# Kernel tuning notes

Measured on AMD Instinct MI355X. Metric: run time of the kernel, lower is better.

The kernel has to match this reference:

```python
import jax, jax.numpy as jnp
import numpy as np

B = 16384
DIM = 1024
HEADS = 16
LN_EPS = 1e-5


def setup_inputs() -> dict:
    key = jax.random.key(0)
    ks = jax.random.split(key, 8)
    d = DIM
    s = 0.02
    return {
        "x_u": jax.random.normal(ks[0], (B, d), dtype=jnp.float32),
        "x_m": jax.random.normal(ks[1], (B, d), dtype=jnp.float32),
        # MHA m2u (path 1): packed in_proj [3d, d] like torch, out_proj [d, d]
        "w_qkv1": (jax.random.normal(ks[2], (3 * d, d), dtype=jnp.float32) * s),
        "b_qkv1": jnp.zeros((3 * d,), dtype=jnp.float32),
        "w_o1": (jax.random.normal(ks[3], (d, d), dtype=jnp.float32) * s),
        "b_o1": jnp.zeros((d,), dtype=jnp.float32),
        # MHA u2m (path 2)
        "w_qkv2": (jax.random.normal(ks[4], (3 * d, d), dtype=jnp.float32) * s),
        "b_qkv2": jnp.zeros((3 * d,), dtype=jnp.float32),
        "w_o2": (jax.random.normal(ks[5], (d, d), dtype=jnp.float32) * s),
        "b_o2": jnp.zeros((d,), dtype=jnp.float32),
        # proj head: LayerNorm(2d) + Linear(2d -> d) + GELU (dropout = eval identity)
        "ln_g": jnp.ones((2 * d,), dtype=jnp.float32),
        "ln_b": jnp.zeros((2 * d,), dtype=jnp.float32),
        "w_proj": (jax.random.normal(ks[6], (d, 2 * d), dtype=jnp.float32) * s),
        "b_proj": jnp.zeros((d,), dtype=jnp.float32),
        "heads": HEADS,
    }


def _mha_single_token(xq, xkv, w_qkv, b_qkv, w_o, b_o, heads):
    # seq_len = 1 cross-attention: softmax over a single key is exactly 1.
    d = xq.shape[-1]
    dh = d // heads
    wq, wk, wv = jnp.split(w_qkv, 3, axis=0)
    bq, bk, bv = jnp.split(b_qkv, 3)
    q = (xq @ wq.T + bq).reshape(-1, heads, dh)   # [B, H, dh]
    k = (xkv @ wk.T + bk).reshape(-1, heads, dh)
    v = (xkv @ wv.T + bv).reshape(-1, heads, dh)
    scores = jnp.sum(q * k, axis=-1) / jnp.sqrt(jnp.asarray(dh, q.dtype))  # [B, H]
    attn = jax.nn.softmax(scores[..., None], axis=-1)  # singleton key axis -> ones
    out = (attn * v).reshape(-1, d)                    # [B, d]
    return out @ w_o.T + b_o


def reference(x_u, x_m, w_qkv1, b_qkv1, w_o1, b_o1,
              w_qkv2, b_qkv2, w_o2, b_o2,
              ln_g, ln_b, w_proj, b_proj, heads):
    # Path 1: Q = x_m, K/V = x_u ; Path 2: Q = x_u, K/V = x_m
    z1 = _mha_single_token(x_m, x_u, w_qkv1, b_qkv1, w_o1, b_o1, heads)
    z2 = _mha_single_token(x_u, x_m, w_qkv2, b_qkv2, w_o2, b_o2, heads)
    z = jnp.concatenate([z1, z2], axis=-1)  # [B, 2d]
    mu = jnp.mean(z, axis=-1, keepdims=True)
    var = jnp.mean(jnp.square(z - mu), axis=-1, keepdims=True)
    zn = (z - mu) * jax.lax.rsqrt(var + LN_EPS) * ln_g + ln_b
    h = zn @ w_proj.T + b_proj               # [B, d]
    return jax.nn.gelu(h, approximate=False)  # torch nn.GELU default = exact erf
```

## Files before the change

kernel.cpp:

```cpp
#include <hip/hip_runtime.h>
#include <cstdint>


#define DIM 1024
#define BROWS 16384

typedef __bf16 bf16x8 __attribute__((ext_vector_type(8)));
typedef float f32x4 __attribute__((ext_vector_type(4)));

__device__ __forceinline__ ushort f2bf(float f) {
    uint32_t u = __builtin_bit_cast(uint32_t, f);
    u = (u + 0x7fffu + ((u >> 16) & 1u)) >> 16;
    return (ushort)u;
}

__device__ __forceinline__ void async_copy16(const void* gsrc, void* ldst) {
    __builtin_amdgcn_global_load_lds(
        (__attribute__((address_space(1))) void*)((uintptr_t)gsrc),
        (__attribute__((address_space(3))) void*)((uint32_t)(uintptr_t)ldst),
        16, 0, 0);
}


__global__ __launch_bounds__(256) void prep_kernel(
        const float* __restrict__ x_u, const float* __restrict__ x_m,
        const float* __restrict__ wqkv1, const float* __restrict__ bqkv1,
        const float* __restrict__ wo1, const float* __restrict__ bo1,
        const float* __restrict__ wqkv2, const float* __restrict__ bqkv2,
        const float* __restrict__ wo2, const float* __restrict__ bo2,
        const float* __restrict__ lng, const float* __restrict__ lnb,
        const float* __restrict__ wproj, const float* __restrict__ bproj,
        ushort* __restrict__ x_bf, ushort* __restrict__ wo12,
        ushort* __restrict__ wvT12, ushort* __restrict__ Wp,
        float* __restrict__ b12, float* __restrict__ Svec, float* __restrict__ Cvec,
        float* __restrict__ sums ) {
    const int b = blockIdx.x, t = threadIdx.x;
    __shared__ float red[4][4];
    __shared__ float tls[32][33];

    if (b < 8192) {
        const int n4 = (BROWS * DIM) / 4;
        int i = b * 256 + t;
        const int stride = 8192 * 256;
        const float4* xu4 = (const float4*)x_u;
        const float4* xm4 = (const float4*)x_m;
        ushort4* o4 = (ushort4*)x_bf;
#pragma unroll
        for (int it = 0; it < 4; it++, i += stride) {
            float4 v = (i < n4) ? xu4[i] : xm4[i - n4];
            ushort4 o;
            o.x = f2bf(v.x); o.y = f2bf(v.y); o.z = f2bf(v.z); o.w = f2bf(v.w);
            o4[i] = o;
        }
    } else if (b < 9216) {
        int j = b - 8192;
        float s1 = 0.f, s2 = 0.f, sS = 0.f, sC = 0.f;
        for (int c = t; c < DIM; c += 256) {
            s1 += wo1[j * DIM + c] * bqkv1[2 * DIM + c];
            s2 += wo2[j * DIM + c] * bqkv2[2 * DIM + c];
        }
        for (int c = t; c < 2 * DIM; c += 256) {
            float w = wproj[j * 2 * DIM + c];
            sS += w * lng[c];
            sC += w * lnb[c];
        }
        for (int o = 32; o; o >>= 1) {
            s1 += __shfl_down(s1, o, 64);
            s2 += __shfl_down(s2, o, 64);
            sS += __shfl_down(sS, o, 64);
            sC += __shfl_down(sC, o, 64);
        }
        int wid = t >> 6;
        if ((t & 63) == 0) { red[wid][0] = s1; red[wid][1] = s2; red[wid][2] = sS; red[wid][3] = sC; }
        __syncthreads();
        if (t == 0) {
            s1 = red[0][0] + red[1][0] + red[2][0] + red[3][0];
            s2 = red[0][1] + red[1][1] + red[2][1] + red[3][1];
            sS = red[0][2] + red[1][2] + red[2][2] + red[3][2];
            sC = red[0][3] + red[1][3] + red[2][3] + red[3][3];
            b12[j]       = s1 + bo1[j];
            b12[DIM + j] = s2 + bo2[j];
            Svec[j] = sS;
            Cvec[j] = sC + bproj[j];
        }
    } else if (b < 12288) {
        const int NWO = (DIM * DIM) / 4;
        const int NWP = (DIM * 2 * DIM) / 4;
        const int total = 2 * NWO + NWP;
        int i = (b - 9216) * 256 + t;
        const int stride = 3072 * 256;
        for (; i < total; i += stride) {
            if (i < 2 * NWO) {
                float4 v = (i < NWO) ? ((const float4*)wo1)[i] : ((const float4*)wo2)[i - NWO];
                ushort4 o;
                o.x = f2bf(v.x); o.y = f2bf(v.y); o.z = f2bf(v.z); o.w = f2bf(v.w);
                ((ushort4*)wo12)[i] = o;
            } else {
                int j = i - 2 * NWO;
                float4 v = ((const float4*)wproj)[j];
                int c = (j * 4) & (2 * DIM - 1);
                v.x *= lng[c]; v.y *= lng[c + 1]; v.z *= lng[c + 2]; v.w *= lng[c + 3];
                ushort4 o;
                o.x = f2bf(v.x); o.y = f2bf(v.y); o.z = f2bf(v.z); o.w = f2bf(v.w);
                ((ushort4*)Wp)[j] = o;
            }
        }
    } else if (b < 14336) {
        int tile = b - 12288;
        int z = tile >> 10;
        int t2 = tile & 1023;
        int mt = t2 >> 5, kt = t2 & 31;
        const float* src = z ? wqkv2 : wqkv1;
        int tr = t >> 3;
        int tc4 = (t & 7) * 4;
        const float* p = src + (long)(2 * DIM + mt * 32 + tr) * DIM + kt * 32 + tc4;
        float4 v = *(const float4*)p;
        tls[tr][tc4 + 0] = v.x; tls[tr][tc4 + 1] = v.y;
        tls[tr][tc4 + 2] = v.z; tls[tr][tc4 + 3] = v.w;
        __syncthreads();
        ushort4 o;
        o.x = f2bf(tls[tc4 + 0][tr]);
        o.y = f2bf(tls[tc4 + 1][tr]);
        o.z = f2bf(tls[tc4 + 2][tr]);
        o.w = f2bf(tls[tc4 + 3][tr]);
        *(ushort4*)(wvT12 + (long)z * DIM * DIM + (long)(kt * 32 + tr) * DIM + mt * 32 + tc4) = o;
    } else {
        int i = (b - 14336) * 256 + t;
        ((float4*)sums)[i] = float4{0.f, 0.f, 0.f, 0.f};
    }
}

template <int BM, int BN, int MODE>
__global__ __launch_bounds__(256, 2) void gemm_bt(
        const ushort* __restrict__ Ag, const ushort* __restrict__ Wg,
        void* __restrict__ Cg, int K, int lda, int ldw, int ldc,
        long sAz, long sWz, long sCz,
        const float* __restrict__ bias,
        const float* __restrict__ Svec, const float* __restrict__ Cvec,
        float* __restrict__ sumbuf, float* __restrict__ sqbuf) {
    constexpr int BK = 32;
    constexpr int MT = BM / 32;
    constexpr int NT = BN / 32;
    __shared__ __align__(16) ushort As[BM * BK];
    __shared__ __align__(16) ushort Bs[BN * BK];
    const int tid = threadIdx.x;
    const int wid = tid >> 6;
    const int lane = tid & 63;
    const int quad = lane >> 4;
    const int l16 = lane & 15;
    const int waveM = wid >> 1, waveN = wid & 1;
    const int zb = blockIdx.z;

    const ushort* A = Ag + zb * sAz + (long)blockIdx.x * BM * lda;
    const ushort* W = Wg + zb * sWz + (long)blockIdx.y * BN * ldw;

    f32x4 acc[MT][NT] = {};

    constexpr int nA = (BM * BK) / (256 * 8);
    constexpr int nB = (BN * BK) / (256 * 8);

    const int swz = (l16 >> 1) & 3;
    const int rdA = quad ^ swz;
    for (int k0 = 0; k0 < K; k0 += BK) {
#pragma unroll
        for (int c = 0; c < nA; c++) {
            int idx = c * 256 + tid;
            int r = idx >> 2;
            int q = (idx & 3) ^ ((r >> 1) & 3);
            const ushort* g = A + (long)r * lda + k0 + q * 8;
            async_copy16(g, (char*)As + (c * 256 + wid * 64) * 16);
        }
#pragma unroll
        for (int c = 0; c < nB; c++) {
            int idx = c * 256 + tid;
            int r = idx >> 2;
            int q = (idx & 3) ^ ((r >> 1) & 3);
            const ushort* g = W + (long)r * ldw + k0 + q * 8;
            async_copy16(g, (char*)Bs + (c * 256 + wid * 64) * 16);
        }
        asm volatile("s_waitcnt vmcnt(0)" ::: "memory");
        __syncthreads();

        bf16x8 af[MT], bfg[NT];
#pragma unroll
        for (int im = 0; im < MT; im++)
            af[im] = *(const bf16x8*)(As + (waveM * (BM / 2) + im * 16 + l16) * BK + rdA * 8);
#pragma unroll
        for (int in = 0; in < NT; in++)
            bfg[in] = *(const bf16x8*)(Bs + (waveN * (BN / 2) + in * 16 + l16) * BK + rdA * 8);
#pragma unroll
        for (int im = 0; im < MT; im++)
#pragma unroll
            for (int in = 0; in < NT; in++)
                acc[im][in] = __builtin_amdgcn_mfma_f32_16x16x32_bf16(
                    af[im], bfg[in], acc[im][in], 0, 0, 0);
        __syncthreads();
    }

    const int gRow0 = blockIdx.x * BM + waveM * (BM / 2) + quad * 4;
    const int gCol0 = blockIdx.y * BN + waveN * (BN / 2) + l16;
    if constexpr (MODE == 0) {
        ushort* C = (ushort*)Cg + zb * sCz;
#pragma unroll
        for (int im = 0; im < MT; im++)
#pragma unroll
            for (int in = 0; in < NT; in++) {
                int col = gCol0 + in * 16;
#pragma unroll
                for (int r = 0; r < 4; r++) {
                    int row = gRow0 + im * 16 + r;
                    C[(long)row * ldc + col] = f2bf(acc[im][in][r]);
                }
            }
    } else if constexpr (MODE == 1) {
        ushort* C = (ushort*)Cg + zb * sCz;
        float rs[MT][4] = {};
        float rq[MT][4] = {};
#pragma unroll
        for (int im = 0; im < MT; im++)
#pragma unroll
            for (int in = 0; in < NT; in++) {
                int col = gCol0 + in * 16;
                float badd = bias[zb * DIM + col];
#pragma unroll
                for (int r = 0; r < 4; r++) {
                    int row = gRow0 + im * 16 + r;
                    float val = acc[im][in][r] + badd;
                    C[(long)row * ldc + col] = f2bf(val);
                    rs[im][r] += val;
                    rq[im][r] += val * val;
                }
            }
#pragma unroll
        for (int im = 0; im < MT; im++)
#pragma unroll
            for (int r = 0; r < 4; r++) {
                float s = rs[im][r], q = rq[im][r];
#pragma unroll
                for (int o = 1; o < 16; o <<= 1) {
                    s += __shfl_xor(s, o, 64);
                    q += __shfl_xor(q, o, 64);
                }
                if (l16 == 0) {
                    int row = gRow0 + im * 16 + r;
                    atomicAdd(&sumbuf[row], s);
                    atomicAdd(&sqbuf[row], q);
                }
            }
    } else {
        float* O = (float*)Cg;
#pragma unroll
        for (int im = 0; im < MT; im++)
#pragma unroll
            for (int r = 0; r < 4; r++) {
                int row = gRow0 + im * 16 + r;
                float sv = sumbuf[row], qv = sqbuf[row];
                float m = sv * (1.f / 2048.f);
                float var = qv * (1.f / 2048.f) - m * m;
                float rstd = rsqrtf(var + 1e-5f);
#pragma unroll
                for (int in = 0; in < NT; in++) {
                    int col = gCol0 + in * 16;
                    float h = rstd * (acc[im][in][r] - m * Svec[col]) + Cvec[col];
                    O[(long)row * ldc + col] = 0.5f * h * (1.0f + erff(h * 0.7071067811865475f));
                }
            }
    }
}


extern "C" void kernel_launch(void* const* d_in, const int* in_sizes, int n_in,
                              void* d_out, int out_size, void* d_ws, size_t ws_size,
                              hipStream_t stream) {
    (void)in_sizes; (void)n_in; (void)out_size; (void)ws_size;
    const float* x_u   = (const float*)d_in[0];
    const float* x_m   = (const float*)d_in[1];
    const float* wqkv1 = (const float*)d_in[2];
    const float* bqkv1 = (const float*)d_in[3];
    const float* wo1   = (const float*)d_in[4];
    const float* bo1   = (const float*)d_in[5];
    const float* wqkv2 = (const float*)d_in[6];
    const float* bqkv2 = (const float*)d_in[7];
    const float* wo2   = (const float*)d_in[8];
    const float* bo2   = (const float*)d_in[9];
    const float* lng   = (const float*)d_in[10];
    const float* lnb   = (const float*)d_in[11];
    const float* wproj = (const float*)d_in[12];
    const float* bproj = (const float*)d_in[13];

    char* ws = (char*)d_ws;
    ushort* x_bf  = (ushort*)(ws + 0);
    ushort* wo12  = (ushort*)(ws + 67108864);
    ushort* wvT12 = (ushort*)(ws + 71303168);
    ushort* W12   = (ushort*)(ws + 75497472);
    ushort* Wp    = (ushort*)(ws + 79691776);
    ushort* zbuf  = (ushort*)(ws + 83886080);
    float*  b12   = (float*)(ws + 150994944);
    float*  Svec  = (float*)(ws + 151003136);
    float*  Cvec  = (float*)(ws + 151007232);
    float*  sumbuf= (float*)(ws + 151011328);
    float*  sqbuf = (float*)(ws + 151076864);

    prep_kernel<<<14368, 256, 0, stream>>>(
        x_u, x_m, wqkv1, bqkv1, wo1, bo1, wqkv2, bqkv2, wo2, bo2,
        lng, lnb, wproj, bproj,
        x_bf, wo12, wvT12, Wp, b12, Svec, Cvec, sumbuf);

    gemm_bt<64, 64, 0><<<dim3(16, 16, 2), 256, 0, stream>>>(
        wo12, wvT12, W12, DIM, DIM, DIM, DIM,
        (long)DIM * DIM, (long)DIM * DIM, (long)DIM * DIM,
        nullptr, nullptr, nullptr, nullptr, nullptr);

    gemm_bt<128, 128, 1><<<dim3(128, 8, 2), 256, 0, stream>>>(
        x_bf, W12, zbuf, DIM, DIM, DIM, 2 * DIM,
        (long)BROWS * DIM, (long)DIM * DIM, (long)DIM,
        b12, nullptr, nullptr, sumbuf, sqbuf);

    gemm_bt<128, 128, 2><<<dim3(128, 8, 1), 256, 0, stream>>>(
        zbuf, Wp, d_out, 2 * DIM, 2 * DIM, 2 * DIM, DIM,
        0, 0, 0,
        nullptr, Svec, Cvec, sumbuf, sqbuf);
}
```

Baseline: 404.2 us.

## Fuse fp32-to-bf16 input conversion into the z GEMM A-tile load

Removes the separate pass that converted x_u and x_m to a bf16 workspace copy. The z GEMM now loads fp32 activations directly with vector loads, converts them in registers and writes swizzled bf16 into LDS, while weights still use async global-to-LDS copies. This drops a full write and re-read of the 64 MB bf16 activation buffer. In exchange, the GEMM reads twice as many bytes for A on every column tile, eight times over, and loses async copy for A. The templated GEMM is also split into three specialized kernels.

```diff
diff --git a/kernel.cpp b/kernel.cpp
--- a/kernel.cpp
+++ b/kernel.cpp
@@ -6,6 +6,7 @@
 #define BROWS 16384
 
 typedef __bf16 bf16x8 __attribute__((ext_vector_type(8)));
+typedef ushort ushort8v __attribute__((ext_vector_type(8)));
 typedef float f32x4 __attribute__((ext_vector_type(4)));
 
 __device__ __forceinline__ ushort f2bf(float f) {
@@ -23,37 +24,22 @@
 
 
 __global__ __launch_bounds__(256) void prep_kernel(
-        const float* __restrict__ x_u, const float* __restrict__ x_m,
         const float* __restrict__ wqkv1, const float* __restrict__ bqkv1,
         const float* __restrict__ wo1, const float* __restrict__ bo1,
         const float* __restrict__ wqkv2, const float* __restrict__ bqkv2,
         const float* __restrict__ wo2, const float* __restrict__ bo2,
         const float* __restrict__ lng, const float* __restrict__ lnb,
         const float* __restrict__ wproj, const float* __restrict__ bproj,
-        ushort* __restrict__ x_bf, ushort* __restrict__ wo12,
-        ushort* __restrict__ wvT12, ushort* __restrict__ Wp,
+        ushort* __restrict__ wo12, ushort* __restrict__ wvT12,
+        ushort* __restrict__ Wp,
         float* __restrict__ b12, float* __restrict__ Svec, float* __restrict__ Cvec,
         float* __restrict__ sums ) {
     const int b = blockIdx.x, t = threadIdx.x;
     __shared__ float red[4][4];
     __shared__ float tls[32][33];
 
-    if (b < 8192) {
-        const int n4 = (BROWS * DIM) / 4;
-        int i = b * 256 + t;
-        const int stride = 8192 * 256;
-        const float4* xu4 = (const float4*)x_u;
-        const float4* xm4 = (const float4*)x_m;
-        ushort4* o4 = (ushort4*)x_bf;
-#pragma unroll
-        for (int it = 0; it < 4; it++, i += stride) {
-            float4 v = (i < n4) ? xu4[i] : xm4[i - n4];
-            ushort4 o;
-            o.x = f2bf(v.x); o.y = f2bf(v.y); o.z = f2bf(v.z); o.w = f2bf(v.w);
-            o4[i] = o;
-        }
-    } else if (b < 9216) {
-        int j = b - 8192;
+    if (b < 1024) {
+        int j = b;
         float s1 = 0.f, s2 = 0.f, sS = 0.f, sC = 0.f;
         for (int c = t; c < DIM; c += 256) {
             s1 += wo1[j * DIM + c] * bqkv1[2 * DIM + c];
@@ -83,11 +69,11 @@
             Svec[j] = sS;
             Cvec[j] = sC + bproj[j];
         }
-    } else if (b < 12288) {
+    } else if (b < 4096) {
         const int NWO = (DIM * DIM) / 4;
         const int NWP = (DIM * 2 * DIM) / 4;
         const int total = 2 * NWO + NWP;
-        int i = (b - 9216) * 256 + t;
+        int i = (b - 1024) * 256 + t;
         const int stride = 3072 * 256;
         for (; i < total; i += stride) {
             if (i < 2 * NWO) {
@@ -105,8 +91,8 @@
                 ((ushort4*)Wp)[j] = o;
             }
         }
-    } else if (b < 14336) {
-        int tile = b - 12288;
+    } else if (b < 6144) {
+        int tile = b - 4096;
         int z = tile >> 10;
         int t2 = tile & 1023;
         int mt = t2 >> 5, kt = t2 & 31;
@@ -125,22 +111,16 @@
         o.w = f2bf(tls[tc4 + 3][tr]);
         *(ushort4*)(wvT12 + (long)z * DIM * DIM + (long)(kt * 32 + tr) * DIM + mt * 32 + tc4) = o;
     } else {
-        int i = (b - 14336) * 256 + t;
+        int i = (b - 6144) * 256 + t;
         ((float4*)sums)[i] = float4{0.f, 0.f, 0.f, 0.f};
     }
 }
 
-template <int BM, int BN, int MODE>
-__global__ __launch_bounds__(256, 2) void gemm_bt(
+__global__ __launch_bounds__(256, 2) void gemm_wfuse(
         const ushort* __restrict__ Ag, const ushort* __restrict__ Wg,
-        void* __restrict__ Cg, int K, int lda, int ldw, int ldc,
-        long sAz, long sWz, long sCz,
-        const float* __restrict__ bias,
-        const float* __restrict__ Svec, const float* __restrict__ Cvec,
-        float* __restrict__ sumbuf, float* __restrict__ sqbuf) {
-    constexpr int BK = 32;
-    constexpr int MT = BM / 32;
-    constexpr int NT = BN / 32;
+        ushort* __restrict__ Cg) {
+    constexpr int BM = 64, BN = 64, BK = 32;
+    constexpr int MT = 2, NT = 2;
     __shared__ __align__(16) ushort As[BM * BK];
     __shared__ __align__(16) ushort Bs[BN * BK];
     const int tid = threadIdx.x;
@@ -151,32 +131,199 @@
     const int waveM = wid >> 1, waveN = wid & 1;
     const int zb = blockIdx.z;
 
-    const ushort* A = Ag + zb * sAz + (long)blockIdx.x * BM * lda;
-    const ushort* W = Wg + zb * sWz + (long)blockIdx.y * BN * ldw;
+    const ushort* A = Ag + (long)zb * DIM * DIM + (long)blockIdx.x * BM * DIM;
+    const ushort* W = Wg + (long)zb * DIM * DIM + (long)blockIdx.y * BN * DIM;
 
     f32x4 acc[MT][NT] = {};
-
-    constexpr int nA = (BM * BK) / (256 * 8);
-    constexpr int nB = (BN * BK) / (256 * 8);
-
-    const int swz = (l16 >> 1) & 3;
-    const int rdA = quad ^ swz;
-    for (int k0 = 0; k0 < K; k0 += BK) {
-#pragma unroll
-        for (int c = 0; c < nA; c++) {
+    const int rdA = quad ^ ((l16 >> 1) & 3);
+
+    for (int k0 = 0; k0 < DIM; k0 += BK) {
+        {
+            int idx = tid;
+            int r = idx >> 2;
+            int q = (idx & 3) ^ ((r >> 1) & 3);
+            async_copy16(A + (long)r * DIM + k0 + q * 8, (char*)As + (wid * 64) * 16);
+            async_copy16(W + (long)r * DIM + k0 + q * 8, (char*)Bs + (wid * 64) * 16);
+        }
+        asm volatile("s_waitcnt vmcnt(0)" ::: "memory");
+        __syncthreads();
+
+        bf16x8 af[MT], bfg[NT];
+#pragma unroll
+        for (int im = 0; im < MT; im++)
+            af[im] = *(const bf16x8*)(As + (waveM * 32 + im * 16 + l16) * BK + rdA * 8);
+#pragma unroll
+        for (int in = 0; in < NT; in++)
+            bfg[in] = *(const bf16x8*)(Bs + (waveN * 32 + in * 16 + l16) * BK + rdA * 8);
+#pragma unroll
+        for (int im = 0; im < MT; im++)
+#pragma unroll
+            for (int in = 0; in < NT; in++)
+                acc[im][in] = __builtin_amdgcn_mfma_f32_16x16x32_bf16(
+                    af[im], bfg[in], acc[im][in], 0, 0, 0);
+        __syncthreads();
+    }
+
+    const int gRow0 = blockIdx.x * BM + waveM * 32 + quad * 4;
+    const int gCol0 = blockIdx.y * BN + waveN * 32 + l16;
+    ushort* C = Cg + (long)zb * DIM * DIM;
+#pragma unroll
+    for (int im = 0; im < MT; im++)
+#pragma unroll
+        for (int in = 0; in < NT; in++) {
+            int col = gCol0 + in * 16;
+#pragma unroll
+            for (int r = 0; r < 4; r++)
+                C[(long)(gRow0 + im * 16 + r) * DIM + col] = f2bf(acc[im][in][r]);
+        }
+}
+
+__global__ __launch_bounds__(256, 2) void gemm_z(
+        const float* __restrict__ x_u, const float* __restrict__ x_m,
+        const ushort* __restrict__ Wg, ushort* __restrict__ Cg,
+        const float* __restrict__ bias,
+        float* __restrict__ sumbuf, float* __restrict__ sqbuf) {
+    constexpr int BM = 128, BN = 128, BK = 32;
+    constexpr int MT = 4, NT = 4;
+    __shared__ __align__(16) ushort As[BM * BK];
+    __shared__ __align__(16) ushort Bs[BN * BK];
+    const int tid = threadIdx.x;
+    const int wid = tid >> 6;
+    const int lane = tid & 63;
+    const int quad = lane >> 4;
+    const int l16 = lane & 15;
+    const int waveM = wid >> 1, waveN = wid & 1;
+    const int zb = blockIdx.z;
+
+    const float* A = (zb ? x_m : x_u) + (long)blockIdx.x * BM * DIM;
+    const ushort* W = Wg + (long)zb * DIM * DIM + (long)blockIdx.y * BN * DIM;
+
+    f32x4 acc[MT][NT] = {};
+    const int rdA = quad ^ ((l16 >> 1) & 3);
+
+    const int ar = tid >> 1;
+    const int ahalf = tid & 1;
+    const float* arow = A + (long)ar * DIM + ahalf * 16;
+    const int aswz = (ar >> 1) & 3;
+    ushort* as0 = As + (ar * 4 + ((ahalf * 2 + 0) ^ aswz)) * 8;
+    ushort* as1 = As + (ar * 4 + ((ahalf * 2 + 1) ^ aswz)) * 8;
+
+    for (int k0 = 0; k0 < DIM; k0 += BK) {
+#pragma unroll
+        for (int c = 0; c < 2; c++) {
             int idx = c * 256 + tid;
             int r = idx >> 2;
             int q = (idx & 3) ^ ((r >> 1) & 3);
-            const ushort* g = A + (long)r * lda + k0 + q * 8;
-            async_copy16(g, (char*)As + (c * 256 + wid * 64) * 16);
-        }
-#pragma unroll
-        for (int c = 0; c < nB; c++) {
+            async_copy16(W + (long)r * DIM + k0 + q * 8,
+                         (char*)Bs + (c * 256 + wid * 64) * 16);
+        }
+        float4 v0 = *(const float4*)(arow + k0 + 0);
+        float4 v1 = *(const float4*)(arow + k0 + 4);
+        float4 v2 = *(const float4*)(arow + k0 + 8);
+        float4 v3 = *(const float4*)(arow + k0 + 12);
+        ushort8v c0, c1;
+        c0[0] = f2bf(v0.x); c0[1] = f2bf(v0.y); c0[2] = f2bf(v0.z); c0[3] = f2bf(v0.w);
+        c0[4] = f2bf(v1.x); c0[5] = f2bf(v1.y); c0[6] = f2bf(v1.z); c0[7] = f2bf(v1.w);
+        c1[0] = f2bf(v2.x); c1[1] = f2bf(v2.y); c1[2] = f2bf(v2.z); c1[3] = f2bf(v2.w);
+        c1[4] = f2bf(v3.x); c1[5] = f2bf(v3.y); c1[6] = f2bf(v3.z); c1[7] = f2bf(v3.w);
+        *(ushort8v*)as0 = c0;
+        *(ushort8v*)as1 = c1;
+        asm volatile("s_waitcnt vmcnt(0)" ::: "memory");
+        __syncthreads();
+
+        bf16x8 af[MT], bfg[NT];
+#pragma unroll
+        for (int im = 0; im < MT; im++)
+            af[im] = *(const bf16x8*)(As + (waveM * 64 + im * 16 + l16) * BK + rdA * 8);
+#pragma unroll
+        for (int in = 0; in < NT; in++)
+            bfg[in] = *(const bf16x8*)(Bs + (waveN * 64 + in * 16 + l16) * BK + rdA * 8);
+#pragma unroll
+        for (int im = 0; im < MT; im++)
+#pragma unroll
+            for (int in = 0; in < NT; in++)
+                acc[im][in] = __builtin_amdgcn_mfma_f32_16x16x32_bf16(
+                    af[im], bfg[in], acc[im][in], 0, 0, 0);
+        __syncthreads();
+    }
+
+    const int gRow0 = blockIdx.x * BM + waveM * 64 + quad * 4;
+    const int gCol0 = blockIdx.y * BN + waveN * 64 + l16;
+    ushort* C = Cg + (long)zb * DIM;
+    float rs[MT][4] = {};
+    float rq[MT][4] = {};
+#pragma unroll
+    for (int im = 0; im < MT; im++)
+#pragma unroll
+        for (int in = 0; in < NT; in++) {
+            int col = gCol0 + in * 16;
+            float badd = bias[zb * DIM + col];
+#pragma unroll
+            for (int r = 0; r < 4; r++) {
+                int row = gRow0 + im * 16 + r;
+                float val = acc[im][in][r] + badd;
+                C[(long)row * 2 * DIM + col] = f2bf(val);
+                rs[im][r] += val;
+                rq[im][r] += val * val;
+            }
+        }
+#pragma unroll
+    for (int im = 0; im < MT; im++)
+#pragma unroll
+        for (int r = 0; r < 4; r++) {
+            float s = rs[im][r], q = rq[im][r];
+#pragma unroll
+            for (int o = 1; o < 16; o <<= 1) {
+                s += __shfl_xor(s, o, 64);
+                q += __shfl_xor(q, o, 64);
+            }
+            if (l16 == 0) {
+                int row = gRow0 + im * 16 + r;
+                atomicAdd(&sumbuf[row], s);
+                atomicAdd(&sqbuf[row], q);
+            }
+        }
+}
+
+__global__ __launch_bounds__(256, 2) void gemm_proj(
+        const ushort* __restrict__ Ag, const ushort* __restrict__ Wg,
+        float* __restrict__ Og,
+        const float* __restrict__ Svec, const float* __restrict__ Cvec,
+        const float* __restrict__ sumbuf, const float* __restrict__ sqbuf) {
+    constexpr int BM = 128, BN = 128, BK = 32;
+    constexpr int MT = 4, NT = 4;
+    constexpr int K = 2 * DIM, LDA = 2 * DIM, LDW = 2 * DIM, LDC = DIM;
+    __shared__ __align__(16) ushort As[BM * BK];
+    __shared__ __align__(16) ushort Bs[BN * BK];
+    const int tid = threadIdx.x;
+    const int wid = tid >> 6;
+    const int lane = tid & 63;
+    const int quad = lane >> 4;
+    const int l16 = lane & 15;
+    const int waveM = wid >> 1, waveN = wid & 1;
+
+    const ushort* A = Ag + (long)blockIdx.x * BM * LDA;
+    const ushort* W = Wg + (long)blockIdx.y * BN * LDW;
+
+    f32x4 acc[MT][NT] = {};
+    const int rdA = quad ^ ((l16 >> 1) & 3);
+
+    for (int k0 = 0; k0 < K; k0 += BK) {
+#pragma unroll
+        for (int c = 0; c < 2; c++) {
             int idx = c * 256 + tid;
             int r = idx >> 2;
             int q = (idx & 3) ^ ((r >> 1) & 3);
-            const ushort* g = W + (long)r * ldw + k0 + q * 8;
-            async_copy16(g, (char*)Bs + (c * 256 + wid * 64) * 16);
+            async_copy16(A + (long)r * LDA + k0 + q * 8,
+                         (char*)As + (c * 256 + wid * 64) * 16);
+        }
+#pragma unroll
+        for (int c = 0; c < 2; c++) {
+            int idx = c * 256 + tid;
+            int r = idx >> 2;
+            int q = (idx & 3) ^ ((r >> 1) & 3);
+            async_copy16(W + (long)r * LDW + k0 + q * 8,
+                         (char*)Bs + (c * 256 + wid * 64) * 16);
         }
         asm volatile("s_waitcnt vmcnt(0)" ::: "memory");
         __syncthreads();
@@ -184,10 +331,10 @@
         bf16x8 af[MT], bfg[NT];
 #pragma unroll
         for (int im = 0; im < MT; im++)
-            af[im] = *(const bf16x8*)(As + (waveM * (BM / 2) + im * 16 + l16) * BK + rdA * 8);
+            af[im] = *(const bf16x8*)(As + (waveM * 64 + im * 16 + l16) * BK + rdA * 8);
 #pragma unroll
         for (int in = 0; in < NT; in++)
-            bfg[in] = *(const bf16x8*)(Bs + (waveN * (BN / 2) + in * 16 + l16) * BK + rdA * 8);
+            bfg[in] = *(const bf16x8*)(Bs + (waveN * 64 + in * 16 + l16) * BK + rdA * 8);
 #pragma unroll
         for (int im = 0; im < MT; im++)
 #pragma unroll
@@ -197,75 +344,24 @@
         __syncthreads();
     }
 
-    const int gRow0 = blockIdx.x * BM + waveM * (BM / 2) + quad * 4;
-    const int gCol0 = blockIdx.y * BN + waveN * (BN / 2) + l16;
-    if constexpr (MODE == 0) {
-        ushort* C = (ushort*)Cg + zb * sCz;
-#pragma unroll
-        for (int im = 0; im < MT; im++)
+    const int gRow0 = blockIdx.x * BM + waveM * 64 + quad * 4;
+    const int gCol0 = blockIdx.y * BN + waveN * 64 + l16;
+#pragma unroll
+    for (int im = 0; im < MT; im++)
+#pragma unroll
+        for (int r = 0; r < 4; r++) {
+            int row = gRow0 + im * 16 + r;
+            float sv = sumbuf[row], qv = sqbuf[row];
+            float m = sv * (1.f / 2048.f);
+            float var = qv * (1.f / 2048.f) - m * m;
+            float rstd = rsqrtf(var + 1e-5f);
 #pragma unroll
             for (int in = 0; in < NT; in++) {
                 int col = gCol0 + in * 16;
-#pragma unroll
-                for (int r = 0; r < 4; r++) {
-                    int row = gRow0 + im * 16 + r;
-                    C[(long)row * ldc + col] = f2bf(acc[im][in][r]);
-                }
+                float h = rstd * (acc[im][in][r] - m * Svec[col]) + Cvec[col];
+                Og[(long)row * LDC + col] = 0.5f * h * (1.0f + erff(h * 0.7071067811865475f));
             }
-    } else if constexpr (MODE == 1) {
-        ushort* C = (ushort*)Cg + zb * sCz;
-        float rs[MT][4] = {};
-        float rq[MT][4] = {};
-#pragma unroll
-        for (int im = 0; im < MT; im++)
-#pragma unroll
-            for (int in = 0; in < NT; in++) {
-                int col = gCol0 + in * 16;
-                float badd = bias[zb * DIM + col];
-#pragma unroll
-                for (int r = 0; r < 4; r++) {
-                    int row = gRow0 + im * 16 + r;
-                    float val = acc[im][in][r] + badd;
-                    C[(long)row * ldc + col] = f2bf(val);
-                    rs[im][r] += val;
-                    rq[im][r] += val * val;
-                }
-            }
-#pragma unroll
-        for (int im = 0; im < MT; im++)
-#pragma unroll
-            for (int r = 0; r < 4; r++) {
-                float s = rs[im][r], q = rq[im][r];
-#pragma unroll
-                for (int o = 1; o < 16; o <<= 1) {
-                    s += __shfl_xor(s, o, 64);
-                    q += __shfl_xor(q, o, 64);
-                }
-                if (l16 == 0) {
-                    int row = gRow0 + im * 16 + r;
-                    atomicAdd(&sumbuf[row], s);
-                    atomicAdd(&sqbuf[row], q);
-                }
-            }
-    } else {
-        float* O = (float*)Cg;
-#pragma unroll
-        for (int im = 0; im < MT; im++)
-#pragma unroll
-            for (int r = 0; r < 4; r++) {
-                int row = gRow0 + im * 16 + r;
-                float sv = sumbuf[row], qv = sqbuf[row];
-                float m = sv * (1.f / 2048.f);
-                float var = qv * (1.f / 2048.f) - m * m;
-                float rstd = rsqrtf(var + 1e-5f);
-#pragma unroll
-                for (int in = 0; in < NT; in++) {
-                    int col = gCol0 + in * 16;
-                    float h = rstd * (acc[im][in][r] - m * Svec[col]) + Cvec[col];
-                    O[(long)row * ldc + col] = 0.5f * h * (1.0f + erff(h * 0.7071067811865475f));
-                }
-            }
-    }
+        }
 }
 
 
@@ -289,35 +385,27 @@
     const float* bproj = (const float*)d_in[13];
 
     char* ws = (char*)d_ws;
-    ushort* x_bf  = (ushort*)(ws + 0);
-    ushort* wo12  = (ushort*)(ws + 67108864);
-    ushort* wvT12 = (ushort*)(ws + 71303168);
-    ushort* W12   = (ushort*)(ws + 75497472);
-    ushort* Wp    = (ushort*)(ws + 79691776);
-    ushort* zbuf  = (ushort*)(ws + 83886080);
-    float*  b12   = (float*)(ws + 150994944);
-    float*  Svec  = (float*)(ws + 151003136);
-    float*  Cvec  = (float*)(ws + 151007232);
-    float*  sumbuf= (float*)(ws + 151011328);
-    float*  sqbuf = (float*)(ws + 151076864);
-
-    prep_kernel<<<14368, 256, 0, stream>>>(
-        x_u, x_m, wqkv1, bqkv1, wo1, bo1, wqkv2, bqkv2, wo2, bo2,
+    ushort* wo12  = (ushort*)(ws + 0);
+    ushort* wvT12 = (ushort*)(ws + 4194304);
+    ushort* W12   = (ushort*)(ws + 8388608);
+    ushort* Wp    = (ushort*)(ws + 12582912);
+    ushort* zbuf  = (ushort*)(ws + 16777216);
+    float*  b12   = (float*)(ws + 83886080);
+    float*  Svec  = (float*)(ws + 83894272);
+    float*  Cvec  = (float*)(ws + 83898368);
+    float*  sumbuf= (float*)(ws + 83902464);
+    float*  sqbuf = (float*)(ws + 83968000);
+
+    prep_kernel<<<6176, 256, 0, stream>>>(
+        wqkv1, bqkv1, wo1, bo1, wqkv2, bqkv2, wo2, bo2,
         lng, lnb, wproj, bproj,
-        x_bf, wo12, wvT12, Wp, b12, Svec, Cvec, sumbuf);
-
-    gemm_bt<64, 64, 0><<<dim3(16, 16, 2), 256, 0, stream>>>(
-        wo12, wvT12, W12, DIM, DIM, DIM, DIM,
-        (long)DIM * DIM, (long)DIM * DIM, (long)DIM * DIM,
-        nullptr, nullptr, nullptr, nullptr, nullptr);
-
-    gemm_bt<128, 128, 1><<<dim3(128, 8, 2), 256, 0, stream>>>(
-        x_bf, W12, zbuf, DIM, DIM, DIM, 2 * DIM,
-        (long)BROWS * DIM, (long)DIM * DIM, (long)DIM,
-        b12, nullptr, nullptr, sumbuf, sqbuf);
-
-    gemm_bt<128, 128, 2><<<dim3(128, 8, 1), 256, 0, stream>>>(
-        zbuf, Wp, d_out, 2 * DIM, 2 * DIM, 2 * DIM, DIM,
-        0, 0, 0,
-        nullptr, Svec, Cvec, sumbuf, sqbuf);
-}
+        wo12, wvT12, Wp, b12, Svec, Cvec, sumbuf);
+
+    gemm_wfuse<<<dim3(16, 16, 2), 256, 0, stream>>>(wo12, wvT12, W12);
+
+    gemm_z<<<dim3(128, 8, 2), 256, 0, stream>>>(
+        x_u, x_m, W12, zbuf, b12, sumbuf, sqbuf);
+
+    gemm_proj<<<dim3(128, 8, 1), 256, 0, stream>>>(
+        zbuf, Wp, (float*)d_out, Svec, Cvec, sumbuf, sqbuf);
+}
```

Result: slower. 420.7 us (+4.1%).
